# Kernel optimization log

Hardware: AMD Instinct MI355X
Metric: run time of the kernel (lower is better)

## Reference

```python
import jax, jax.numpy as jnp
import numpy as np

# dims
B, CIN, H, W = 64, 96, 28, 28
E = 4            # num_experts
EXPAND = 6
HID = CIN * EXPAND   # 576
K = 5
STRIDE = 1
PAD = K // 2
RED = max(1, int(CIN * 0.25))      # SE reduced dim = 24
RHID = max(16, CIN // 4)           # routing hidden = 24
COUT = 96
EPS = 1e-3


def setup_inputs() -> dict:
    key = jax.random.key(0)
    ks = jax.random.split(key, 12)
    rn = lambda k, shape, s=0.05: jax.random.normal(k, shape, jnp.float32) * s
    return dict(
        x=jax.random.normal(ks[0], (B, CIN, H, W), jnp.float32),
        # routing net: Linear(CIN->RHID) + ReLU + Linear(RHID->E)
        r_w1=rn(ks[1], (RHID, CIN)), r_b1=jnp.zeros((RHID,), jnp.float32),
        r_w2=rn(ks[2], (E, RHID)), r_b2=jnp.zeros((E,), jnp.float32),
        # expand 1x1 conv (no bias)
        exp_w=rn(ks[3], (HID, CIN)),
        bn1_g=jnp.ones((HID,), jnp.float32), bn1_b=jnp.zeros((HID,), jnp.float32),
        bn1_m=jnp.zeros((HID,), jnp.float32), bn1_v=jnp.ones((HID,), jnp.float32),
        # MoE depthwise expert kernels [E, HID, K, K]
        dw_w=rn(ks[4], (E, HID, K, K)),
        bn2_g=jnp.ones((HID,), jnp.float32), bn2_b=jnp.zeros((HID,), jnp.float32),
        bn2_m=jnp.zeros((HID,), jnp.float32), bn2_v=jnp.ones((HID,), jnp.float32),
        # squeeze-excitation 1x1 convs (with bias)
        se_w1=rn(ks[5], (RED, HID)), se_b1=jnp.zeros((RED,), jnp.float32),
        se_w2=rn(ks[6], (HID, RED)), se_b2=jnp.zeros((HID,), jnp.float32),
        # MoE pointwise expert kernels [E, COUT, HID]
        pw_w=rn(ks[7], (E, COUT, HID)),
        bn3_g=jnp.ones((COUT,), jnp.float32), bn3_b=jnp.zeros((COUT,), jnp.float32),
        bn3_m=jnp.zeros((COUT,), jnp.float32), bn3_v=jnp.ones((COUT,), jnp.float32),
    )


def _bn(y, g, b, m, v):
    sh = (1, -1, 1, 1)
    inv = g.reshape(sh) * jax.lax.rsqrt(v.reshape(sh) + EPS)
    return (y - m.reshape(sh)) * inv + b.reshape(sh)


def _dwconv_per_sample(x, kernels):
    # x [b,c,h,w], kernels [b,c,k,k] -> per-sample depthwise conv
    c = x.shape[1]
    def one(xi, wi):
        return jax.lax.conv_general_dilated(
            xi[None], wi[:, None],  # [1,c,h,w], [c,1,k,k]
            window_strides=(STRIDE, STRIDE),
            padding=[(PAD, PAD), (PAD, PAD)],
            feature_group_count=c,
            dimension_numbers=('NCHW', 'OIHW', 'NCHW'))[0]
    return jax.vmap(one)(x, kernels)


def reference(x, r_w1, r_b1, r_w2, r_b2, exp_w,
              bn1_g, bn1_b, bn1_m, bn1_v, dw_w,
              bn2_g, bn2_b, bn2_m, bn2_v,
              se_w1, se_b1, se_w2, se_b2, pw_w,
              bn3_g, bn3_b, bn3_m, bn3_v):
    silu = jax.nn.silu
    # routing: global avg pool -> MLP -> softmax (temperature = 1.0)
    pool = x.mean(axis=(2, 3))                          # [b, cin]
    hdn = jax.nn.relu(pool @ r_w1.T + r_b1)             # [b, rhid]
    logits = (hdn @ r_w2.T + r_b2).astype(jnp.float32)  # [b, E]
    rw = jax.nn.softmax(logits, axis=-1).astype(x.dtype)
    # expand 1x1 conv + BN + SiLU
    out = jnp.einsum('oc,bchw->bohw', exp_w, x)         # [b, hid, h, w]
    out = silu(_bn(out, bn1_g, bn1_b, bn1_m, bn1_v))
    # MoE depthwise: aggregate per-sample kernels, per-sample depthwise conv
    kern = jnp.einsum('be,eckl->bckl', rw, dw_w)        # [b, hid, k, k]
    out = _dwconv_per_sample(out, kern)
    out = silu(_bn(out, bn2_g, bn2_b, bn2_m, bn2_v))
    # squeeze-excitation
    s = out.mean(axis=(2, 3))                           # [b, hid]
    z = silu(s @ se_w1.T + se_b1)                       # [b, red]
    sc = jax.nn.sigmoid(z @ se_w2.T + se_b2)            # [b, hid]
    out = out * sc[:, :, None, None]
    # MoE pointwise projection: per-sample 1x1 conv weights
    wpw = jnp.einsum('be,eoc->boc', rw, pw_w)           # [b, cout, hid]
    out = jnp.einsum('boc,bchw->bohw', wpw, out)        # [b, cout, h, w]
    out = _bn(out, bn3_g, bn3_b, bn3_m, bn3_v)
    # residual (stride==1, cin==cout); stochastic depth is identity in eval
    return x + out
```

## Files before the change

kernel.cpp:

```cpp
#include <hip/hip_runtime.h>
#include <hip/hip_bf16.h>
#include <math.h>

#define B 64
#define CIN 96
#define HH 28
#define WW 28
#define NPIX 784
#define E 4
#define HID 576
#define RED 24
#define RHID 24
#define COUT 96
#define EPS 1e-3f

typedef __attribute__((ext_vector_type(8))) short short8v;
typedef __attribute__((ext_vector_type(4))) float f32x4;

__device__ __forceinline__ float sigmoidf_(float v) { return 1.0f / (1.0f + __expf(-v)); }

__device__ __forceinline__ unsigned short f2bf(float v) {
    __hip_bfloat16 h = __float2bfloat16(v);
    return *reinterpret_cast<unsigned short*>(&h);
}

__device__ __forceinline__ float bf2f(unsigned short u) {
    unsigned int w = ((unsigned int)u) << 16;
    return *reinterpret_cast<float*>(&w);
}

__global__ __launch_bounds__(256) void k_pool_wcvt(const float* __restrict__ x, float* __restrict__ pool,
                                                   const float* __restrict__ w, unsigned short* __restrict__ wb) {
    if (blockIdx.x < 1536) {
        int row = blockIdx.x * 4 + (threadIdx.x >> 6);
        int lane = threadIdx.x & 63;
        const float4* xr = reinterpret_cast<const float4*>(x + (size_t)row * NPIX);
        float s = 0.f;
        for (int i = lane; i < 196; i += 64) {
            float4 v = xr[i];
            s += v.x + v.y + v.z + v.w;
        }
#pragma unroll
        for (int off = 32; off > 0; off >>= 1) s += __shfl_down(s, off);
        if (lane == 0) pool[row] = s * (1.0f / NPIX);
    } else {
        int i = (blockIdx.x - 1536) * 256 + threadIdx.x;
        wb[i] = f2bf(w[i]);
    }
}

__global__ __launch_bounds__(256) void k_mlp(const float* __restrict__ pool,
                                             const float* __restrict__ r_w1, const float* __restrict__ r_b1,
                                             const float* __restrict__ r_w2, const float* __restrict__ r_b2,
                                             float* __restrict__ rw) {
    __shared__ float w1[RHID * CIN];
    __shared__ float b1s[RHID];
    __shared__ float w2[E * RHID];
    __shared__ float b2s[E];
    __shared__ float pl[B * CIN];
    int tid = threadIdx.x;
    for (int i = tid; i < RHID * CIN; i += 256) w1[i] = r_w1[i];
    if (tid < RHID) b1s[tid] = r_b1[tid];
    if (tid < E * RHID) w2[tid] = r_w2[tid];
    if (tid < E) b2s[tid] = r_b2[tid];
    for (int i = tid; i < B * CIN; i += 256) pl[i] = pool[i];
    __syncthreads();
    if (tid < B) {
        const float* p = pl + tid * CIN;
        float hdn[RHID];
#pragma unroll
        for (int r = 0; r < RHID; ++r) {
            float a = b1s[r];
            for (int c = 0; c < CIN; ++c) a += p[c] * w1[r * CIN + c];
            hdn[r] = fmaxf(a, 0.f);
        }
        float lg[E];
        float mx = -1e30f;
#pragma unroll
        for (int e = 0; e < E; ++e) {
            float a = b2s[e];
#pragma unroll
            for (int r = 0; r < RHID; ++r) a += hdn[r] * w2[e * RHID + r];
            lg[e] = a;
            mx = fmaxf(mx, a);
        }
        float den = 0.f;
#pragma unroll
        for (int e = 0; e < E; ++e) { lg[e] = __expf(lg[e] - mx); den += lg[e]; }
#pragma unroll
        for (int e = 0; e < E; ++e) rw[tid * E + e] = lg[e] / den;
    }
}

__global__ __launch_bounds__(256) void k_expand_mfma(
    const float* __restrict__ x, const unsigned short* __restrict__ w_bf,
    const float* __restrict__ bn1_g, const float* __restrict__ bn1_b,
    const float* __restrict__ bn1_m, const float* __restrict__ bn1_v,
    __hip_bfloat16* __restrict__ hid) {
    int nc = blockIdx.x;
    int b = blockIdx.y;
    int tid = threadIdx.x;
    int lane = tid & 63, wv = tid >> 6;
    int col = lane & 15, g = lane >> 4;
    __shared__ unsigned short xt[96 * 116];
    __shared__ float inv1s[HID], sh1s[HID];

    for (int i = tid; i < HID; i += 256) {
        float inv = bn1_g[i] * rsqrtf(bn1_v[i] + EPS);
        inv1s[i] = inv;
        sh1s[i] = bn1_b[i] - bn1_m[i] * inv;
    }
    const float* xb = x + (size_t)b * CIN * NPIX + nc * 112;
    for (int i = tid; i < 96 * 28; i += 256) {
        int c = i / 28, q = i % 28;
        float4 v = *reinterpret_cast<const float4*>(&xb[c * NPIX + q * 4]);
        ushort4 s;
        s.x = f2bf(v.x); s.y = f2bf(v.y); s.z = f2bf(v.z); s.w = f2bf(v.w);
        *reinterpret_cast<ushort4*>(&xt[c * 116 + q * 4]) = s;
    }

    const short8v* wv8 = reinterpret_cast<const short8v*>(w_bf);
    short8v af[9][3];
#pragma unroll
    for (int mi = 0; mi < 9; ++mi) {
#pragma unroll
        for (int kk = 0; kk < 3; ++kk)
            af[mi][kk] = wv8[(((wv * 9 + mi) * 16 + col) * 96 + kk * 32 + 8 * g) >> 3];
    }
    __syncthreads();

    for (int nf = 0; nf < 7; ++nf) {
        int pcol = nf * 16 + col;
        short8v bfr[3];
#pragma unroll
        for (int kk = 0; kk < 3; ++kk) {
            int k0 = kk * 32 + 8 * g;
#pragma unroll
            for (int j = 0; j < 8; ++j) bfr[kk][j] = (short)xt[(k0 + j) * 116 + pcol];
        }
        int px = nc * 112 + pcol;
#pragma unroll
        for (int mi = 0; mi < 9; ++mi) {
            int mb = (wv * 9 + mi) * 16;
            f32x4 acc = {0.f, 0.f, 0.f, 0.f};
#pragma unroll
            for (int kk = 0; kk < 3; ++kk)
                acc = __builtin_amdgcn_mfma_f32_16x16x32_bf16(af[mi][kk], bfr[kk], acc, 0, 0, 0);
#pragma unroll
            for (int r = 0; r < 4; ++r) {
                int oc = mb + 4 * g + r;
                float t = acc[r] * inv1s[oc] + sh1s[oc];
                float u = t * sigmoidf_(t);
                hid[((size_t)b * HID + oc) * NPIX + px] = __float2bfloat16(u);
            }
        }
    }
}

#define CT 16
#define RSF 33
#define PCSF 1063
__global__ __launch_bounds__(448) void k_dw(
    __hip_bfloat16* __restrict__ hid, const float* __restrict__ rw,
    const float* __restrict__ dw_w,
    const float* __restrict__ bn2_g, const float* __restrict__ bn2_b,
    const float* __restrict__ bn2_m, const float* __restrict__ bn2_v,
    float* __restrict__ s_out) {
    int ct = blockIdx.x;
    int b = blockIdx.y;
    int tid = threadIdx.x;
    int cb = ct * CT;
    __shared__ float PF[CT * PCSF];
    __shared__ float kl[CT][25];
    __shared__ float ssum[CT];
    __hip_bfloat16* hb = hid + ((size_t)b * HID + cb) * NPIX;

    for (int i = tid; i < CT * PCSF; i += 448) PF[i] = 0.f;
    if (tid < CT) ssum[tid] = 0.f;
    __syncthreads();

    int ci = tid / 28, w = tid - ci * 28;
    {
        const unsigned int* src = reinterpret_cast<const unsigned int*>(hb) + ci * (NPIX / 2) + w * 14;
        float* dst = PF + ci * PCSF + (w + 2) * RSF + 2;
#pragma unroll
        for (int d = 0; d < 14; ++d) {
            unsigned int v = src[d];
            dst[2 * d]     = bf2f((unsigned short)(v & 0xffffu));
            dst[2 * d + 1] = bf2f((unsigned short)(v >> 16));
        }
    }
    {
        float rwl[E];
#pragma unroll
        for (int e = 0; e < E; ++e) rwl[e] = rw[b * E + e];
        for (int i = tid; i < CT * 25; i += 448) {
            int c2 = i / 25, j = i % 25;
            int c = cb + c2;
            float a = 0.f;
#pragma unroll
            for (int e = 0; e < E; ++e) a += rwl[e] * dw_w[((size_t)e * HID + c) * 25 + j];
            kl[c2][j] = a * (bn2_g[c] * rsqrtf(bn2_v[c] + EPS));
        }
    }
    __syncthreads();

    const float* Pc = PF + ci * PCSF + w;
    float k[25];
#pragma unroll
    for (int j = 0; j < 25; ++j) k[j] = kl[ci][j];
    int c = cb + ci;
    float inv2 = bn2_g[c] * rsqrtf(bn2_v[c] + EPS);
    float sh2 = bn2_b[c] - bn2_m[c] * inv2;
    unsigned short* hout = reinterpret_cast<unsigned short*>(hb) + ci * NPIX + w;

    float win[5][5];
#pragma unroll
    for (int i = 0; i < 5; ++i)
#pragma unroll
        for (int j = 0; j < 5; ++j) win[i][j] = Pc[i * RSF + j];

    float csum = 0.f;
#pragma unroll
    for (int h = 0; h < HH; ++h) {
        float o = 0.f;
#pragma unroll
        for (int i = 0; i < 5; ++i)
#pragma unroll
            for (int j = 0; j < 5; ++j) o += win[i][j] * k[i * 5 + j];
        float t = o + sh2;
        float u = t * sigmoidf_(t);
        csum += u;
        hout[h * WW] = f2bf(u);
        if (h < HH - 1) {
#pragma unroll
            for (int i = 0; i < 4; ++i)
#pragma unroll
                for (int j = 0; j < 5; ++j) win[i][j] = win[i + 1][j];
#pragma unroll
            for (int j = 0; j < 5; ++j) win[4][j] = Pc[(h + 5) * RSF + j];
        }
    }
    atomicAdd(&ssum[ci], csum);
    __syncthreads();
    if (tid < CT) s_out[(size_t)b * HID + cb + tid] = ssum[tid] * (1.0f / NPIX);
}

__global__ __launch_bounds__(256) void k_se_wpw(
    const float* __restrict__ s, const float* __restrict__ se_w1,
    const float* __restrict__ se_b1, const float* __restrict__ se_w2,
    const float* __restrict__ se_b2, const float* __restrict__ rw,
    const float* __restrict__ pw_w,
    const float* __restrict__ bn3_g, const float* __restrict__ bn3_v,
    unsigned short* __restrict__ wpw) {
    int seg = blockIdx.x;
    int b = blockIdx.y;
    int tid = threadIdx.x;
    __shared__ float sl[HID];
    __shared__ float zl[RED];
    __shared__ float scl[HID];
    for (int i = tid; i < HID; i += 256) sl[i] = s[(size_t)b * HID + i];
    __syncthreads();
    if (tid < RED * 8) {
        int r = tid >> 3, l = tid & 7;
        float a = 0.f;
        for (int c = l; c < HID; c += 8) a += sl[c] * se_w1[r * HID + c];
        a += __shfl_down(a, 4, 8);
        a += __shfl_down(a, 2, 8);
        a += __shfl_down(a, 1, 8);
        if (l == 0) {
            a += se_b1[r];
            zl[r] = a * sigmoidf_(a);
        }
    }
    __syncthreads();
    for (int c = tid; c < HID; c += 256) {
        float a = se_b2[c];
#pragma unroll
        for (int r = 0; r < RED; ++r) a += zl[r] * se_w2[c * RED + r];
        scl[c] = sigmoidf_(a);
    }
    __syncthreads();
    float rwl[E];
#pragma unroll
    for (int e = 0; e < E; ++e) rwl[e] = rw[b * E + e];
    unsigned short* wb = wpw + (size_t)b * COUT * HID;
    for (int i = tid; i < 16 * HID; i += 256) {
        int o = seg * 16 + i / HID, c = i % HID;
        float a = 0.f;
#pragma unroll
        for (int e = 0; e < E; ++e) a += rwl[e] * pw_w[((size_t)e * COUT + o) * HID + c];
        float inv3 = bn3_g[o] * rsqrtf(bn3_v[o] + EPS);
        wb[o * HID + c] = f2bf(a * inv3 * scl[c]);
    }
}

__global__ __launch_bounds__(448) void k_pw_mfma(
    const __hip_bfloat16* __restrict__ hid, const unsigned short* __restrict__ wpw,
    const float* __restrict__ x,
    const float* __restrict__ bn3_g, const float* __restrict__ bn3_b,
    const float* __restrict__ bn3_m, const float* __restrict__ bn3_v,
    float* __restrict__ out) {
    int nc = blockIdx.x;
    int b = blockIdx.y;
    int tid = threadIdx.x;
    int lane = tid & 63, nf = tid >> 6;
    int col = lane & 15, g = lane >> 4;
    __shared__ unsigned short Wl[96 * 104];
    __shared__ unsigned short Ht[96 * 116];
    __shared__ float inv3s[COUT], sh3s[COUT];
    if (tid < COUT) {
        float inv = bn3_g[tid] * rsqrtf(bn3_v[tid] + EPS);
        inv3s[tid] = inv;
        sh3s[tid] = bn3_b[tid] - bn3_m[tid] * inv;
    }
    const unsigned short* hb = (const unsigned short*)hid + (size_t)b * HID * NPIX + nc * 112;
    const unsigned short* wb = wpw + (size_t)b * COUT * HID;
    f32x4 acc[6];
#pragma unroll
    for (int m = 0; m < 6; ++m) acc[m] = (f32x4){0.f, 0.f, 0.f, 0.f};

    for (int ks = 0; ks < 6; ++ks) {
        __syncthreads();
        for (int i = tid; i < 96 * 12; i += 448) {
            int m = i / 12, q = i % 12;
            *(uint4*)&Wl[m * 104 + 8 * q] = *(const uint4*)&wb[m * HID + ks * 96 + 8 * q];
        }
        for (int i = tid; i < 96 * 28; i += 448) {
            int k = i / 28, q = i % 28;
            *(uint2*)&Ht[k * 116 + 4 * q] = *(const uint2*)&hb[((size_t)(ks * 96 + k)) * NPIX + 4 * q];
        }
        __syncthreads();
#pragma unroll
        for (int kk = 0; kk < 3; ++kk) {
            int k0 = kk * 32 + 8 * g;
            short8v bfr;
#pragma unroll
            for (int j = 0; j < 8; ++j) bfr[j] = (short)Ht[(k0 + j) * 116 + nf * 16 + col];
#pragma unroll
            for (int m = 0; m < 6; ++m) {
                short8v af = *(const short8v*)&Wl[(m * 16 + col) * 104 + kk * 32 + 8 * g];
                acc[m] = __builtin_amdgcn_mfma_f32_16x16x32_bf16(af, bfr, acc[m], 0, 0, 0);
            }
        }
    }
    int px = nc * 112 + nf * 16 + col;
#pragma unroll
    for (int m = 0; m < 6; ++m) {
#pragma unroll
        for (int r = 0; r < 4; ++r) {
            int oc = m * 16 + 4 * g + r;
            size_t off = ((size_t)b * COUT + oc) * NPIX + px;
            out[off] = acc[m][r] + sh3s[oc] + x[off];
        }
    }
}

extern "C" void kernel_launch(void* const* d_in, const int* in_sizes, int n_in,
                              void* d_out, int out_size, void* d_ws, size_t ws_size,
                              hipStream_t stream) {
    const float* x     = (const float*)d_in[0];
    const float* r_w1  = (const float*)d_in[1];
    const float* r_b1  = (const float*)d_in[2];
    const float* r_w2  = (const float*)d_in[3];
    const float* r_b2  = (const float*)d_in[4];
    const float* exp_w = (const float*)d_in[5];
    const float* bn1_g = (const float*)d_in[6];
    const float* bn1_b = (const float*)d_in[7];
    const float* bn1_m = (const float*)d_in[8];
    const float* bn1_v = (const float*)d_in[9];
    const float* dw_w  = (const float*)d_in[10];
    const float* bn2_g = (const float*)d_in[11];
    const float* bn2_b = (const float*)d_in[12];
    const float* bn2_m = (const float*)d_in[13];
    const float* bn2_v = (const float*)d_in[14];
    const float* se_w1 = (const float*)d_in[15];
    const float* se_b1 = (const float*)d_in[16];
    const float* se_w2 = (const float*)d_in[17];
    const float* se_b2 = (const float*)d_in[18];
    const float* pw_w  = (const float*)d_in[19];
    const float* bn3_g = (const float*)d_in[20];
    const float* bn3_b = (const float*)d_in[21];
    const float* bn3_m = (const float*)d_in[22];
    const float* bn3_v = (const float*)d_in[23];
    float* out = (float*)d_out;

    char* ws = (char*)d_ws;
    float* rw                 = (float*)(ws + 0);
    float* pool               = (float*)(ws + 1024);
    float* s                  = (float*)(ws + 26624);
    unsigned short* exp_w_bf  = (unsigned short*)(ws + 174336);
    unsigned short* wpw_bf    = (unsigned short*)(ws + 285184);
    __hip_bfloat16* hid       = (__hip_bfloat16*)(ws + 7363328);

    k_pool_wcvt<<<1536 + 216, 256, 0, stream>>>(x, pool, exp_w, exp_w_bf);
    k_mlp<<<1, 256, 0, stream>>>(pool, r_w1, r_b1, r_w2, r_b2, rw);
    k_expand_mfma<<<dim3(7, B), 256, 0, stream>>>(x, exp_w_bf, bn1_g, bn1_b, bn1_m, bn1_v, hid);
    k_dw<<<dim3(36, B), 448, 0, stream>>>(hid, rw, dw_w, bn2_g, bn2_b, bn2_m, bn2_v, s);
    k_se_wpw<<<dim3(6, B), 256, 0, stream>>>(s, se_w1, se_b1, se_w2, se_b2, rw, pw_w, bn3_g, bn3_v, wpw_bf);
    k_pw_mfma<<<dim3(7, B), 448, 0, stream>>>(hid, wpw_bf, x, bn3_g, bn3_b, bn3_m, bn3_v, out);
}
```

Before: 295.9 us.

## Transpose LDS tiles to pixel-major for vector MFMA B-fragment loads

The expand and pointwise kernels now stage their activation tiles in LDS in pixel-major order (row stride 104), transposing while loading from global. Each MFMA B fragment then comes from one 16-byte LDS read instead of eight scalar 2-byte reads. The global loads become per-element strided reads across channels instead of float4/uint2 vector loads, which can weaken coalescing. The depthwise kernel also splits its 25-term accumulation into five independent chains to shorten the dependency chain, and changes the padded plane stride PCSF.

```diff
diff --git a/kernel.cpp b/kernel.cpp
--- a/kernel.cpp
+++ b/kernel.cpp
@@ -102,7 +102,7 @@
     int tid = threadIdx.x;
     int lane = tid & 63, wv = tid >> 6;
     int col = lane & 15, g = lane >> 4;
-    __shared__ unsigned short xt[96 * 116];
+    __shared__ unsigned short xt2[112 * 104];
     __shared__ float inv1s[HID], sh1s[HID];
 
     for (int i = tid; i < HID; i += 256) {
@@ -111,12 +111,15 @@
         sh1s[i] = bn1_b[i] - bn1_m[i] * inv;
     }
     const float* xb = x + (size_t)b * CIN * NPIX + nc * 112;
-    for (int i = tid; i < 96 * 28; i += 256) {
-        int c = i / 28, q = i % 28;
-        float4 v = *reinterpret_cast<const float4*>(&xb[c * NPIX + q * 4]);
+    for (int i = tid; i < 24 * 112; i += 256) {
+        int cg = i / 112, px = i % 112;
+        const float* xp = xb + 4 * cg * NPIX + px;
         ushort4 s;
-        s.x = f2bf(v.x); s.y = f2bf(v.y); s.z = f2bf(v.z); s.w = f2bf(v.w);
-        *reinterpret_cast<ushort4*>(&xt[c * 116 + q * 4]) = s;
+        s.x = f2bf(xp[0]);
+        s.y = f2bf(xp[NPIX]);
+        s.z = f2bf(xp[2 * NPIX]);
+        s.w = f2bf(xp[3 * NPIX]);
+        *reinterpret_cast<ushort4*>(&xt2[px * 104 + 4 * cg]) = s;
     }
 
     const short8v* wv8 = reinterpret_cast<const short8v*>(w_bf);
@@ -133,11 +136,8 @@
         int pcol = nf * 16 + col;
         short8v bfr[3];
 #pragma unroll
-        for (int kk = 0; kk < 3; ++kk) {
-            int k0 = kk * 32 + 8 * g;
-#pragma unroll
-            for (int j = 0; j < 8; ++j) bfr[kk][j] = (short)xt[(k0 + j) * 116 + pcol];
-        }
+        for (int kk = 0; kk < 3; ++kk)
+            bfr[kk] = *(const short8v*)&xt2[pcol * 104 + kk * 32 + 8 * g];
         int px = nc * 112 + pcol;
 #pragma unroll
         for (int mi = 0; mi < 9; ++mi) {
@@ -159,7 +159,7 @@
 
 #define CT 16
 #define RSF 33
-#define PCSF 1063
+#define PCSF 1084
 __global__ __launch_bounds__(448) void k_dw(
     __hip_bfloat16* __restrict__ hid, const float* __restrict__ rw,
     const float* __restrict__ dw_w,
@@ -223,12 +223,17 @@
     float csum = 0.f;
 #pragma unroll
     for (int h = 0; h < HH; ++h) {
-        float o = 0.f;
-#pragma unroll
-        for (int i = 0; i < 5; ++i)
-#pragma unroll
-            for (int j = 0; j < 5; ++j) o += win[i][j] * k[i * 5 + j];
-        float t = o + sh2;
+        float o0 = win[0][0] * k[0], o1 = win[1][0] * k[5], o2 = win[2][0] * k[10],
+              o3 = win[3][0] * k[15], o4 = win[4][0] * k[20];
+#pragma unroll
+        for (int j = 1; j < 5; ++j) {
+            o0 += win[0][j] * k[j];
+            o1 += win[1][j] * k[5 + j];
+            o2 += win[2][j] * k[10 + j];
+            o3 += win[3][j] * k[15 + j];
+            o4 += win[4][j] * k[20 + j];
+        }
+        float t = ((o0 + o1) + (o2 + o3)) + (o4 + sh2);
         float u = t * sigmoidf_(t);
         csum += u;
         hout[h * WW] = f2bf(u);
@@ -307,7 +312,7 @@
     int lane = tid & 63, nf = tid >> 6;
     int col = lane & 15, g = lane >> 4;
     __shared__ unsigned short Wl[96 * 104];
-    __shared__ unsigned short Ht[96 * 116];
+    __shared__ unsigned short Ht2[112 * 104];
     __shared__ float inv3s[COUT], sh3s[COUT];
     if (tid < COUT) {
         float inv = bn3_g[tid] * rsqrtf(bn3_v[tid] + EPS);
@@ -326,17 +331,20 @@
             int m = i / 12, q = i % 12;
             *(uint4*)&Wl[m * 104 + 8 * q] = *(const uint4*)&wb[m * HID + ks * 96 + 8 * q];
         }
-        for (int i = tid; i < 96 * 28; i += 448) {
-            int k = i / 28, q = i % 28;
-            *(uint2*)&Ht[k * 116 + 4 * q] = *(const uint2*)&hb[((size_t)(ks * 96 + k)) * NPIX + 4 * q];
+        for (int i = tid; i < 24 * 112; i += 448) {
+            int kg = i / 112, px = i % 112;
+            const unsigned short* hk = hb + (size_t)(ks * 96 + 4 * kg) * NPIX + px;
+            ushort4 s;
+            s.x = hk[0];
+            s.y = hk[NPIX];
+            s.z = hk[2 * NPIX];
+            s.w = hk[3 * NPIX];
+            *reinterpret_cast<ushort4*>(&Ht2[px * 104 + 4 * kg]) = s;
         }
         __syncthreads();
 #pragma unroll
         for (int kk = 0; kk < 3; ++kk) {
-            int k0 = kk * 32 + 8 * g;
-            short8v bfr;
-#pragma unroll
-            for (int j = 0; j < 8; ++j) bfr[j] = (short)Ht[(k0 + j) * 116 + nf * 16 + col];
+            short8v bfr = *(const short8v*)&Ht2[(nf * 16 + col) * 104 + kk * 32 + 8 * g];
 #pragma unroll
             for (int m = 0; m < 6; ++m) {
                 short8v af = *(const short8v*)&Wl[(m * 16 + col) * 104 + kk * 32 + 8 * g];
```

New measurement: 293.5 us. About the same (-0.8%).
